# Kernel tuning notes

Hardware: AMD Instinct MI355X
Metric: run time of the kernel (lower is better)

## Reference

```python
import jax, jax.numpy as jnp
import numpy as np

# Direction order matches shifted_c_map[:, :, i] = shift(c_map, Directable[TL_table[i]])
# TL_table = [lower_right, down, lower_left, right, left, upper_right, up, upper_left]
DIRS = [(1, 1), (0, 1), (-1, 1), (1, 0), (-1, 0), (1, -1), (0, -1), (-1, -1)]


def _shift(img, dx, dy):
    """Zero-filled pixel shift of [B,C,H,W]; equivalent to the bmm against the
    one-hot translation matrices in the torch code (dx=1 -> shift right, dy=1 -> shift down)."""
    H, W = img.shape[-2], img.shape[-1]
    if dx == 1:
        img = jnp.pad(img, ((0, 0), (0, 0), (0, 0), (1, 0)))[..., :W]
    elif dx == -1:
        img = jnp.pad(img, ((0, 0), (0, 0), (0, 0), (0, 1)))[..., 1:]
    if dy == 1:
        img = jnp.pad(img, ((0, 0), (0, 0), (1, 0), (0, 0)))[..., :H, :]
    elif dy == -1:
        img = jnp.pad(img, ((0, 0), (0, 0), (0, 1), (0, 0)))[..., 1:, :]
    return img


def setup_inputs() -> dict:
    key = jax.random.key(0)
    k1, k2, k3 = jax.random.split(key, 3)
    B, C, H, W = 16, 2, 512, 512
    c_map = jax.random.normal(k1, (B, C, H, W), dtype=jnp.float32)
    target = jax.random.randint(k2, (B, H, W), 0, 2, dtype=jnp.int64)
    con_target = jax.random.randint(k3, (B, 8, H, W), 0, 2).astype(jnp.float32)
    return {"c_map": c_map, "target": target, "con_target": con_target}


def reference(c_map, target, con_target):
    # Bilater_voting: all 8 copies along dim 2 are identical to c_map, so
    # shifted_c_map[:, :, i] = shift(c_map, DIRS[i]).
    shifted = jnp.stack([_shift(c_map, dx, dy) for dx, dy in DIRS], axis=2)  # [B,C,8,H,W]
    vote_out = c_map[:, :, None, :, :] * shifted                              # bimap [B,C,8,H,W]

    # CrossEntropyLoss(c_map, target)
    logp = jax.nn.log_softmax(c_map, axis=1)                                  # [B,C,H,W]
    ce_l = -jnp.mean(jnp.take_along_axis(logp, target[:, None, :, :], axis=1))

    # edge_loss(bimap.squeeze(1)=bimap since C>1, con_target)
    p = jax.nn.softmax(vote_out, axis=1)                                      # softmax over class dim
    sum_conn = 2.0 * con_target                                               # concat-dup then sum over dim 1
    edge = ((sum_conn < 8.0) & (sum_conn > 0.0)).astype(c_map.dtype)          # [B,8,H,W]
    pred_mask_min = jnp.min(p, axis=1) * edge                                 # [B,8,H,W]
    # F.binary_cross_entropy(p, 0) = mean(-log(1-p)), log clamped at -100 like torch
    minloss = jnp.mean(-jnp.clip(jnp.log1p(-pred_mask_min), -100.0, None))

    return 0.2 * minloss + 0.8 * ce_l
```

## Files before the change

### kernel.cpp

```cpp
#include <hip/hip_runtime.h>

#define BB 16
#define HH 512
#define WW 512
#define HWSZ (HH * WW)
#define NPIX ((double)(BB * HH * WW))
#define NBLOCKS 4096

#define L2E 1.4426950408889634f
#define LN2 0.6931471805599453

__device__ __forceinline__ float hw_exp2(float x) { return __builtin_amdgcn_exp2f(x); }
__device__ __forceinline__ float hw_log2(float x) { return __builtin_amdgcn_logf(x); }


__global__ __launch_bounds__(256, 4) void bicon_main(
    const float* __restrict__ cmap,
    const int*   __restrict__ target,
    const float* __restrict__ con,
    double* __restrict__ partials)
{
    constexpr int dxs[8] = {1, 0, -1, 1, -1, 1, 0, -1};
    constexpr int dys[8] = {1, 1,  1, 0,  0, -1, -1, -1};

    const int tid = blockIdx.x * blockDim.x + threadIdx.x;
    const int w4 = (tid & 127) * 4;
    const int h  = (tid >> 7) & 511;
    const int b  = tid >> 16;

    const float* __restrict__ c0p = cmap + (size_t)(b * 2) * HWSZ;
    const float* __restrict__ c1p = c0p + HWSZ;
    const size_t roff = (size_t)h * WW + w4;

    const bool upok = (h > 0);
    const bool dnok = (h < HH - 1);
    const bool lok  = (w4 > 0);
    const bool rok  = (w4 < WW - 4);

    const float4 C0 = *(const float4*)(c0p + roff);
    const float4 C1 = *(const float4*)(c1p + roff);
    const int4   TG = *(const int4*)(target + (size_t)b * HWSZ + roff);

    float4 U0 = {0,0,0,0}, U1 = {0,0,0,0}, D0 = {0,0,0,0}, D1 = {0,0,0,0};
    if (upok) { U0 = *(const float4*)(c0p + roff - WW); U1 = *(const float4*)(c1p + roff - WW); }
    if (dnok) { D0 = *(const float4*)(c0p + roff + WW); D1 = *(const float4*)(c1p + roff + WW); }

    const float* cb = con + (size_t)(b * 8) * HWSZ + roff;
    float4 CV[8];
    #pragma unroll
    for (int i = 0; i < 8; ++i)
        CV[i] = *(const float4*)(cb + (size_t)i * HWSZ);

    const float u0l = (upok && lok) ? c0p[roff - WW - 1] : 0.0f;
    const float u0r = (upok && rok) ? c0p[roff - WW + 4] : 0.0f;
    const float u1l = (upok && lok) ? c1p[roff - WW - 1] : 0.0f;
    const float u1r = (upok && rok) ? c1p[roff - WW + 4] : 0.0f;
    const float m0l = lok ? c0p[roff - 1] : 0.0f;
    const float m0r = rok ? c0p[roff + 4] : 0.0f;
    const float m1l = lok ? c1p[roff - 1] : 0.0f;
    const float m1r = rok ? c1p[roff + 4] : 0.0f;
    const float d0l = (dnok && lok) ? c0p[roff + WW - 1] : 0.0f;
    const float d0r = (dnok && rok) ? c0p[roff + WW + 4] : 0.0f;
    const float d1l = (dnok && lok) ? c1p[roff + WW - 1] : 0.0f;
    const float d1r = (dnok && rok) ? c1p[roff + WW + 4] : 0.0f;

    const float n0[3][6] = {{u0l, U0.x, U0.y, U0.z, U0.w, u0r},
                            {m0l, C0.x, C0.y, C0.z, C0.w, m0r},
                            {d0l, D0.x, D0.y, D0.z, D0.w, d0r}};
    const float n1[3][6] = {{u1l, U1.x, U1.y, U1.z, U1.w, u1r},
                            {m1l, C1.x, C1.y, C1.z, C1.w, m1r},
                            {d1l, D1.x, D1.y, D1.z, D1.w, d1r}};

    const float cc0[4] = {C0.x, C0.y, C0.z, C0.w};
    const float cc1[4] = {C1.x, C1.y, C1.z, C1.w};
    const int   tt[4]  = {TG.x, TG.y, TG.z, TG.w};

    float acc_min_l2 = 0.0f;
    float acc_ce_l2  = 0.0f;
    float acc_ce_lin = 0.0f;

    #pragma unroll
    for (int j = 0; j < 4; ++j) {
        const float dl = cc0[j] - cc1[j];
        acc_ce_l2 += hw_log2(1.0f + hw_exp2(-fabsf(dl) * L2E));
        const float lin = (tt[j] == 0) ? -dl : dl;
        acc_ce_lin += fmaxf(lin, 0.0f);
    }

    #pragma unroll
    for (int i = 0; i < 8; ++i) {
        const int rr = 1 - dys[i];
        const float cts[4] = {CV[i].x, CV[i].y, CV[i].z, CV[i].w};
        #pragma unroll
        for (int j = 0; j < 4; ++j) {
            const int cidx = j - dxs[i] + 1;
            const float d = fmaf(cc0[j], n0[rr][cidx], -(cc1[j] * n1[rr][cidx]));
            const float term = hw_log2(1.0f + hw_exp2(-fabsf(d) * L2E));
            acc_min_l2 = fmaf(term, cts[j], acc_min_l2);
        }
    }

    double contrib = (0.8 / NPIX) * ((double)acc_ce_lin + LN2 * (double)acc_ce_l2)
                   + (0.2 * LN2 / (8.0 * NPIX)) * (double)acc_min_l2;

    #pragma unroll
    for (int off = 32; off > 0; off >>= 1)
        contrib += __shfl_down(contrib, off);

    __shared__ double sm[4];
    const int lane = threadIdx.x & 63;
    const int wid  = threadIdx.x >> 6;
    if (lane == 0) sm[wid] = contrib;
    __syncthreads();
    if (threadIdx.x == 0)
        partials[blockIdx.x] = sm[0] + sm[1] + sm[2] + sm[3];
}

__global__ __launch_bounds__(256) void bicon_finalize(
    const double* __restrict__ partials, int n, float* __restrict__ out)
{
    double s = 0.0;
    for (int i = threadIdx.x; i < n; i += blockDim.x) s += partials[i];
    #pragma unroll
    for (int off = 32; off > 0; off >>= 1)
        s += __shfl_down(s, off);

    __shared__ double sm[4];
    const int lane = threadIdx.x & 63;
    const int wid  = threadIdx.x >> 6;
    if (lane == 0) sm[wid] = s;
    __syncthreads();
    if (threadIdx.x == 0)
        out[0] = (float)(sm[0] + sm[1] + sm[2] + sm[3]);
}

extern "C" void kernel_launch(void* const* d_in, const int* in_sizes, int n_in,
                              void* d_out, int out_size, void* d_ws, size_t ws_size,
                              hipStream_t stream) {
    const float* cmap   = (const float*)d_in[0];
    const int*   target = (const int*)d_in[1];
    const float* con    = (const float*)d_in[2];
    float* out = (float*)d_out;
    double* partials = (double*)d_ws;

    bicon_main<<<NBLOCKS, 256, 0, stream>>>(cmap, target, con, partials);
    bicon_finalize<<<1, 256, 0, stream>>>(partials, NBLOCKS, out);
}
```

Baseline: 225.6 us.

## Stage cmap tile with halo in LDS for stencil neighbor reuse

Each block now handles an 8x128 pixel tile. It cooperatively loads both cmap class planes, plus a one-row and four-column halo, into shared memory with float4 loads, zero-filling outside the image. Neighbor values for the 8 shifted products are then read from LDS instead of through 12 scalar and 4 extra vector global loads per thread. This removes redundant global and L1 traffic, at the cost of a block-wide barrier and extra LDS reads. The dominant con_target stream is unchanged.

New measurement: 229.9 us. Within noise of the previous version (+1.9%).

```diff
diff --git a/kernel.cpp b/kernel.cpp
--- a/kernel.cpp
+++ b/kernel.cpp
@@ -5,7 +5,15 @@
 #define WW 512
 #define HWSZ (HH * WW)
 #define NPIX ((double)(BB * HH * WW))
-#define NBLOCKS 4096
+
+#define TW 128
+#define TH 8
+#define NWT (WW / TW)
+#define NHT (HH / TH)
+#define NBLOCKS (BB * NWT * NHT)
+
+#define LROW 136
+#define NSLOT 680
 
 #define L2E 1.4426950408889634f
 #define LN2 0.6931471805599453
@@ -23,54 +31,56 @@
     constexpr int dxs[8] = {1, 0, -1, 1, -1, 1, 0, -1};
     constexpr int dys[8] = {1, 1,  1, 0,  0, -1, -1, -1};
 
-    const int tid = blockIdx.x * blockDim.x + threadIdx.x;
-    const int w4 = (tid & 127) * 4;
-    const int h  = (tid >> 7) & 511;
-    const int b  = tid >> 16;
+    __shared__ float sh[2 * 10 * LROW];
 
-    const float* __restrict__ c0p = cmap + (size_t)(b * 2) * HWSZ;
-    const float* __restrict__ c1p = c0p + HWSZ;
-    const size_t roff = (size_t)h * WW + w4;
+    const int t   = threadIdx.x;
+    const int bid = blockIdx.x;
+    const int wt = bid & (NWT - 1);
+    const int rt = (bid >> 2) & (NHT - 1);
+    const int b  = bid >> 8;
+    const int w0 = wt * TW;
+    const int h0 = rt * TH;
 
-    const bool upok = (h > 0);
-    const bool dnok = (h < HH - 1);
-    const bool lok  = (w4 > 0);
-    const bool rok  = (w4 < WW - 4);
-
-    const float4 C0 = *(const float4*)(c0p + roff);
-    const float4 C1 = *(const float4*)(c1p + roff);
-    const int4   TG = *(const int4*)(target + (size_t)b * HWSZ + roff);
-
-    float4 U0 = {0,0,0,0}, U1 = {0,0,0,0}, D0 = {0,0,0,0}, D1 = {0,0,0,0};
-    if (upok) { U0 = *(const float4*)(c0p + roff - WW); U1 = *(const float4*)(c1p + roff - WW); }
-    if (dnok) { D0 = *(const float4*)(c0p + roff + WW); D1 = *(const float4*)(c1p + roff + WW); }
+    const int qrow = t >> 5;
+    const int qcol = t & 31;
+    const int h = h0 + qrow;
+    const int w = w0 + qcol * 4;
+    const size_t roff = (size_t)h * WW + w;
 
     const float* cb = con + (size_t)(b * 8) * HWSZ + roff;
     float4 CV[8];
     #pragma unroll
     for (int i = 0; i < 8; ++i)
         CV[i] = *(const float4*)(cb + (size_t)i * HWSZ);
+    const int4 TG = *(const int4*)(target + (size_t)b * HWSZ + roff);
 
-    const float u0l = (upok && lok) ? c0p[roff - WW - 1] : 0.0f;
-    const float u0r = (upok && rok) ? c0p[roff - WW + 4] : 0.0f;
-    const float u1l = (upok && lok) ? c1p[roff - WW - 1] : 0.0f;
-    const float u1r = (upok && rok) ? c1p[roff - WW + 4] : 0.0f;
-    const float m0l = lok ? c0p[roff - 1] : 0.0f;
-    const float m0r = rok ? c0p[roff + 4] : 0.0f;
-    const float m1l = lok ? c1p[roff - 1] : 0.0f;
-    const float m1r = rok ? c1p[roff + 4] : 0.0f;
-    const float d0l = (dnok && lok) ? c0p[roff + WW - 1] : 0.0f;
-    const float d0r = (dnok && rok) ? c0p[roff + WW + 4] : 0.0f;
-    const float d1l = (dnok && lok) ? c1p[roff + WW - 1] : 0.0f;
-    const float d1r = (dnok && rok) ? c1p[roff + WW + 4] : 0.0f;
+    const float* c0base = cmap + (size_t)(b * 2) * HWSZ;
+    #pragma unroll
+    for (int k = 0; k < 3; ++k) {
+        const int s = t + k * 256;
+        if (s < NSLOT) {
+            const int cls = (s >= 340) ? 1 : 0;
+            const int s2  = s - cls * 340;
+            const int row = s2 / 34;
+            const int qc  = s2 - row * 34;
+            const int g   = h0 - 1 + row;
+            const int gw  = w0 - 4 + qc * 4;
+            float4 v = {0.0f, 0.0f, 0.0f, 0.0f};
+            if (g >= 0 && g < HH && gw >= 0 && gw < WW)
+                v = *(const float4*)(c0base + (size_t)cls * HWSZ + (size_t)g * WW + gw);
+            ((float4*)sh)[s] = v;
+        }
+    }
+    __syncthreads();
 
-    const float n0[3][6] = {{u0l, U0.x, U0.y, U0.z, U0.w, u0r},
-                            {m0l, C0.x, C0.y, C0.z, C0.w, m0r},
-                            {d0l, D0.x, D0.y, D0.z, D0.w, d0r}};
-    const float n1[3][6] = {{u1l, U1.x, U1.y, U1.z, U1.w, u1r},
-                            {m1l, C1.x, C1.y, C1.z, C1.w, m1r},
-                            {d1l, D1.x, D1.y, D1.z, D1.w, d1r}};
+    const float* s0 = sh;
+    const float* s1 = sh + 10 * LROW;
+    const int r = qrow + 1;
+    const int c = qcol * 4 + 4;
 
+    const int off1 = r * LROW + c;
+    const float4 C0 = *(const float4*)(s0 + off1);
+    const float4 C1 = *(const float4*)(s1 + off1);
     const float cc0[4] = {C0.x, C0.y, C0.z, C0.w};
     const float cc1[4] = {C1.x, C1.y, C1.z, C1.w};
     const int   tt[4]  = {TG.x, TG.y, TG.z, TG.w};
@@ -88,15 +98,24 @@
     }
 
     #pragma unroll
-    for (int i = 0; i < 8; ++i) {
-        const int rr = 1 - dys[i];
-        const float cts[4] = {CV[i].x, CV[i].y, CV[i].z, CV[i].w};
+    for (int wr = 0; wr < 3; ++wr) {
+        const int o = (r - 1 + wr) * LROW + c;
+        const float4 A0 = *(const float4*)(s0 + o);
+        const float4 A1 = *(const float4*)(s1 + o);
+        const float n0[6] = {s0[o - 1], A0.x, A0.y, A0.z, A0.w, s0[o + 4]};
+        const float n1[6] = {s1[o - 1], A1.x, A1.y, A1.z, A1.w, s1[o + 4]};
+
         #pragma unroll
-        for (int j = 0; j < 4; ++j) {
-            const int cidx = j - dxs[i] + 1;
-            const float d = fmaf(cc0[j], n0[rr][cidx], -(cc1[j] * n1[rr][cidx]));
-            const float term = hw_log2(1.0f + hw_exp2(-fabsf(d) * L2E));
-            acc_min_l2 = fmaf(term, cts[j], acc_min_l2);
+        for (int i = 0; i < 8; ++i) {
+            if (dys[i] != 1 - wr) continue;
+            const float cts[4] = {CV[i].x, CV[i].y, CV[i].z, CV[i].w};
+            #pragma unroll
+            for (int j = 0; j < 4; ++j) {
+                const int cidx = j - dxs[i] + 1;
+                const float d = fmaf(cc0[j], n0[cidx], -(cc1[j] * n1[cidx]));
+                const float term = hw_log2(1.0f + hw_exp2(-fabsf(d) * L2E));
+                acc_min_l2 = fmaf(term, cts[j], acc_min_l2);
+            }
         }
     }
 
```
